# Kernel optimization log

Measured on AMD Instinct MI355X. Metric: run time of the kernel, lower is better.

Reference implementation:

```python
import jax, jax.numpy as jnp
import numpy as np

B, S, D, H = 2, 2048, 1024, 16
HD = D // H


def setup_inputs() -> dict:
    key = jax.random.key(0)
    ks = jax.random.split(key, 7)
    mk = lambda k, shape, scale=1.0: (jax.random.normal(k, shape, dtype=jnp.float32) * scale)
    w_scale = 1.0 / np.sqrt(D)  # ~nn.Linear init scale
    return {
        "query": mk(ks[0], (B, S, D)),
        "key": mk(ks[1], (B, S, D)),
        "value": mk(ks[2], (B, S, D)),
        "Wq": mk(ks[3], (D, D), w_scale),
        "Wk": mk(ks[4], (D, D), w_scale),
        "Wv": mk(ks[5], (D, D), w_scale),
        "Wo": mk(ks[6], (D, D), w_scale),
    }


def reference(query, key, value, Wq, Wk, Wv, Wo):
    # torch nn.Linear(bias=False): y = x @ W.T, W is (out, in)
    def proj(x, W):
        y = jnp.einsum('bsd,ed->bse', x, W)          # [B, S, D]
        return y.reshape(x.shape[0], x.shape[1], H, HD).transpose(0, 2, 1, 3)  # [B, H, S, HD]

    Q = proj(query, Wq)
    K = proj(key, Wk)
    V = proj(value, Wv)

    # NOTE: original scales by sqrt(embedding_size), not sqrt(head_dim)
    scale = 1.0 / jnp.sqrt(jnp.asarray(D, dtype=Q.dtype))
    scores = jnp.einsum('bhqd,bhkd->bhqk', Q, K) * scale   # [B, H, Q, K]
    attn = jax.nn.softmax(scores, axis=-1)
    ctx = jnp.einsum('bhqk,bhkd->bhqd', attn, V)           # [B, H, Q, HD]
    ctx = ctx.transpose(0, 2, 1, 3).reshape(query.shape[0], query.shape[1], D)
    return jnp.einsum('bsd,ed->bse', ctx, Wo)
```

## Files before the change

### kernel.cpp

```cpp
#include <hip/hip_runtime.h>
#include <hip/hip_bf16.h>


typedef __bf16 bf16x8 __attribute__((ext_vector_type(8)));
typedef float f32x2 __attribute__((ext_vector_type(2)));
typedef float f32x4 __attribute__((ext_vector_type(4)));
typedef float f32x8 __attribute__((ext_vector_type(8)));
typedef float f32x16 __attribute__((ext_vector_type(16)));
typedef int i32x4 __attribute__((ext_vector_type(4)));

static constexpr int Bb = 2, Ss = 2048, Dd = 1024, Hh = 16, HDd = 64;
static constexpr int Mtot = Bb * Ss;

__global__ __launch_bounds__(256) void cast_all(
    const float* __restrict__ a0, const float* __restrict__ a1, const float* __restrict__ a2,
    const float* __restrict__ a3, const float* __restrict__ a4, const float* __restrict__ a5,
    const float* __restrict__ a6, __hip_bfloat16* __restrict__ d0, __hip_bfloat16* __restrict__ d1,
    __hip_bfloat16* __restrict__ d2, __hip_bfloat16* __restrict__ d3,
    __hip_bfloat16* __restrict__ d4, __hip_bfloat16* __restrict__ d5,
    __hip_bfloat16* __restrict__ d6, int nact8, int nw8) {
  const float* src;
  __hip_bfloat16* dst;
  int n8;
  switch (blockIdx.y) {
    case 0: src = a0; dst = d0; n8 = nact8; break;
    case 1: src = a1; dst = d1; n8 = nact8; break;
    case 2: src = a2; dst = d2; n8 = nact8; break;
    case 3: src = a3; dst = d3; n8 = nw8; break;
    case 4: src = a4; dst = d4; n8 = nw8; break;
    case 5: src = a5; dst = d5; n8 = nw8; break;
    default: src = a6; dst = d6; n8 = nw8; break;
  }
  int i = blockIdx.x * 256 + threadIdx.x;
  if (i >= n8) return;
  const float4* s4 = (const float4*)src + (size_t)i * 2;
  float4 a = s4[0], b = s4[1];
  union { __hip_bfloat16 h[8]; int4 v; } u;
  u.h[0] = __float2bfloat16(a.x); u.h[1] = __float2bfloat16(a.y);
  u.h[2] = __float2bfloat16(a.z); u.h[3] = __float2bfloat16(a.w);
  u.h[4] = __float2bfloat16(b.x); u.h[5] = __float2bfloat16(b.y);
  u.h[6] = __float2bfloat16(b.z); u.h[7] = __float2bfloat16(b.w);
  ((int4*)dst)[i] = u.v;
}

#define BM 128
#define BK 64

__device__ __forceinline__ void gload_lds16(const void* g, void* l) {
  __builtin_amdgcn_global_load_lds((const __attribute__((address_space(1))) unsigned*)g,
                                   (__attribute__((address_space(3))) unsigned*)l, 16, 0, 0);
}

__device__ __forceinline__ void storeC(float* C, size_t idx, float v) { C[idx] = v; }
__device__ __forceinline__ void storeC(__hip_bfloat16* C, size_t idx, float v) {
  C[idx] = __float2bfloat16(v);
}

template <typename OutT, int BNT>
__device__ __forceinline__ void gemm_bt_body(const __hip_bfloat16* __restrict__ A,
                                             const __hip_bfloat16* __restrict__ Bw,
                                             OutT* __restrict__ C, int K, int N, float cscale) {
  constexpr int NTC = BNT / 32;
  __shared__ __hip_bfloat16 As[BM * BK];
  __shared__ __hip_bfloat16 Bs[BNT * BK];
  const int tid = threadIdx.x;
  const int lane = tid & 63;
  const int wid = tid >> 6;
  const int wm = (wid >> 1) * 64;
  const int wn = (wid & 1) * (BNT / 2);
  const int bm = blockIdx.x, bn = blockIdx.y;
  const int l15 = lane & 15;
  const int lhi = lane >> 4;

  f32x4 zero = {0.f, 0.f, 0.f, 0.f};
  f32x4 acc[4][NTC];
#pragma unroll
  for (int i = 0; i < 4; ++i)
#pragma unroll
    for (int j = 0; j < NTC; ++j) acc[i][j] = zero;

  const size_t abase = (size_t)(bm * BM) * K;
  const size_t bbase = (size_t)(bn * BNT) * K;

  for (int k0 = 0; k0 < K; k0 += BK) {
#pragma unroll
    for (int p = 0; p < 4; ++p) {
      int c = p * 256 + tid;
      int row = c >> 3;
      int col = (c & 7) * 8;
      gload_lds16(A + abase + (size_t)row * K + k0 + col, (char*)As + c * 16);
    }
#pragma unroll
    for (int p = 0; p < BNT / 32; ++p) {
      int c = p * 256 + tid;
      int row = c >> 3;
      int col = (c & 7) * 8;
      gload_lds16(Bw + bbase + (size_t)row * K + k0 + col, (char*)Bs + c * 16);
    }
    __syncthreads();
#pragma unroll
    for (int kk = 0; kk < 2; ++kk) {
      bf16x8 af[4], bfr[NTC];
#pragma unroll
      for (int mt = 0; mt < 4; ++mt)
        af[mt] = *(const bf16x8*)&As[(wm + mt * 16 + l15) * BK + kk * 32 + lhi * 8];
#pragma unroll
      for (int nt = 0; nt < NTC; ++nt)
        bfr[nt] = *(const bf16x8*)&Bs[(wn + nt * 16 + l15) * BK + kk * 32 + lhi * 8];
#pragma unroll
      for (int mt = 0; mt < 4; ++mt)
#pragma unroll
        for (int nt = 0; nt < NTC; ++nt)
          acc[mt][nt] = __builtin_amdgcn_mfma_f32_16x16x32_bf16(af[mt], bfr[nt], acc[mt][nt], 0, 0, 0);
    }
    __syncthreads();
  }

#pragma unroll
  for (int mt = 0; mt < 4; ++mt)
#pragma unroll
    for (int r = 0; r < 4; ++r) {
      int row = bm * BM + wm + mt * 16 + lhi * 4 + r;
#pragma unroll
      for (int nt = 0; nt < NTC; ++nt) {
        int col = bn * BNT + wn + nt * 16 + l15;
        storeC(C, (size_t)row * N + col, acc[mt][nt][r] * cscale);
      }
    }
}

__global__ __launch_bounds__(256) void qkv_proj(
    const __hip_bfloat16* __restrict__ xq, const __hip_bfloat16* __restrict__ xk,
    const __hip_bfloat16* __restrict__ xv, const __hip_bfloat16* __restrict__ wq,
    const __hip_bfloat16* __restrict__ wk, const __hip_bfloat16* __restrict__ wv,
    __hip_bfloat16* __restrict__ Qp, __hip_bfloat16* __restrict__ Kp,
    __hip_bfloat16* __restrict__ Vp) {
  const __hip_bfloat16* A;
  const __hip_bfloat16* W;
  __hip_bfloat16* C;
  float cs = 1.0f;
  if (blockIdx.z == 0) { A = xq; W = wq; C = Qp; cs = 0.04508422f; }
  else if (blockIdx.z == 1) { A = xk; W = wk; C = Kp; }
  else { A = xv; W = wv; C = Vp; }
  gemm_bt_body<__hip_bfloat16, 128>(A, W, C, Dd, Dd, cs);
}

__global__ __launch_bounds__(256) void out_proj(const __hip_bfloat16* __restrict__ ctx,
                                                const __hip_bfloat16* __restrict__ wo,
                                                float* __restrict__ out) {
  gemm_bt_body<float, 64>(ctx, wo, out, Dd, Dd, 1.0f);
}

__global__ __launch_bounds__(256) void transpose_v(const __hip_bfloat16* __restrict__ Vp,
                                                   __hip_bfloat16* __restrict__ Vt) {
  __shared__ __hip_bfloat16 T[64][72];
  const int tid = threadIdx.x;
  const int s0 = blockIdx.x * 64;
  const int bh = blockIdx.y;
  const int b = bh >> 4, h = bh & 15;
  const __hip_bfloat16* src = Vp + (size_t)b * Ss * Dd + (size_t)h * HDd;
#pragma unroll
  for (int p = 0; p < 2; ++p) {
    int id = p * 256 + tid;
    int r = id >> 3, c8 = (id & 7) * 8;
    *(int4*)&T[r][c8] = *(const int4*)(src + (size_t)(s0 + r) * Dd + c8);
  }
  __syncthreads();
#pragma unroll
  for (int p = 0; p < 2; ++p) {
    int id = p * 256 + tid;
    int d = id >> 3, s8 = (id & 7) * 8;
    union { int4 v; __hip_bfloat16 hh[8]; } u;
#pragma unroll
    for (int j = 0; j < 8; ++j) u.hh[j] = T[s8 + j][d];
    *(int4*)(Vt + ((size_t)bh * HDd + d) * Ss + s0 + s8) = u.v;
  }
}

__global__ __launch_bounds__(256) void attn_kernel(const __hip_bfloat16* __restrict__ Qp,
                                                   const __hip_bfloat16* __restrict__ Kp,
                                                   const __hip_bfloat16* __restrict__ Vt,
                                                   float* __restrict__ Po,
                                                   float* __restrict__ Pl) {
  constexpr int HT = 16;
  __shared__ __align__(16) __hip_bfloat16 Ks[3][64 * 64];
  __shared__ __align__(16) __hip_bfloat16 Vs[3][64 * 64];

  const int tid = threadIdx.x;
  const int lane = tid & 63, wid = tid >> 6;
  const int l31 = lane & 31;
  const bool hih = (lane >= 32);
  const int lhi2 = hih ? 1 : 0;

  const int bid = blockIdx.x;
  const int w = (bid & 7) * 128 + (bid >> 3);
  const int bh = w >> 5;
  const int qblk = (w & 31) >> 1;
  const int half = w & 1;

  const int b = bh >> 4, h = bh & 15;
  const size_t head_off = (size_t)b * Ss * Dd + (size_t)h * HDd;
  const size_t vt_off = (size_t)bh * HDd * Ss;
  const int qrow = qblk * 128 + wid * 32 + l31;

  bf16x8 qf[4];
#pragma unroll
  for (int ksd = 0; ksd < 4; ++ksd)
    qf[ksd] = *(const bf16x8*)(Qp + head_off + (size_t)qrow * Dd + ksd * 16 + lhi2 * 8);

  const i32x4 onesbits = {0x3F803F80, 0x3F803F80, 0x3F803F80, 0x3F803F80};
  const bf16x8 ones = __builtin_bit_cast(bf16x8, onesbits);

  f32x16 o[2], ol;
#pragma unroll
  for (int db = 0; db < 2; ++db)
#pragma unroll
    for (int r = 0; r < 16; ++r) o[db][r] = 0.f;
#pragma unroll
  for (int r = 0; r < 16; ++r) ol[r] = 0.f;

  auto stage = [&](int buf, int kv0) {
#pragma unroll
    for (int p = 0; p < 2; ++p) {
      int c = p * 256 + tid;
      int row = c >> 3;
      int sch = (c & 7) ^ (row & 7);
      gload_lds16(Kp + head_off + (size_t)(kv0 + row) * Dd + sch * 8,
                  (char*)&Ks[buf][0] + c * 16);
      gload_lds16(Vt + vt_off + (size_t)row * Ss + kv0 + sch * 8,
                  (char*)&Vs[buf][0] + c * 16);
    }
  };

  const int t0 = half * HT;
  stage(0, (t0 + 0) * 64);
  stage(1, (t0 + 1) * 64);
  asm volatile("s_waitcnt vmcnt(4)" ::: "memory");
  __builtin_amdgcn_s_barrier();
  __builtin_amdgcn_sched_barrier(0);

  int cur = 0;
  for (int t = 0; t < HT; ++t) {
    int sbuf = cur + 2; if (sbuf >= 3) sbuf -= 3;
    if (t + 2 < HT) stage(sbuf, (t0 + t + 2) * 64);

    const char* kbase = (const char*)&Ks[cur][0];
    bf16x8 kfrag[2][4];
#pragma unroll
    for (int kb = 0; kb < 2; ++kb) {
      int row = kb * 32 + l31;
#pragma unroll
      for (int ksd = 0; ksd < 4; ++ksd)
        kfrag[kb][ksd] = *(const bf16x8*)(kbase + row * 128 +
                                          (((ksd * 2 + lhi2) ^ (row & 7)) << 4));
    }
    f32x16 st[2];
#pragma unroll
    for (int kb = 0; kb < 2; ++kb)
#pragma unroll
      for (int r = 0; r < 16; ++r) st[kb][r] = 0.f;
    __builtin_amdgcn_s_setprio(1);
#pragma unroll
    for (int kb = 0; kb < 2; ++kb)
#pragma unroll
      for (int ksd = 0; ksd < 4; ++ksd)
        st[kb] = __builtin_amdgcn_mfma_f32_32x32x16_bf16(kfrag[kb][ksd], qf[ksd], st[kb], 0, 0, 0);
    __builtin_amdgcn_s_setprio(0);

#pragma unroll
    for (int kb = 0; kb < 2; ++kb)
#pragma unroll
      for (int r = 0; r < 16; ++r) st[kb][r] = exp2f(st[kb][r]);

    int cpk[2][4][2];
#pragma unroll
    for (int kb = 0; kb < 2; ++kb)
#pragma unroll
      for (int g = 0; g < 4; ++g)
#pragma unroll
        for (int i = 0; i < 2; ++i) {
          int rr;
          float lo = st[kb][g * 4 + 2 * i], hi = st[kb][g * 4 + 2 * i + 1];
          asm("v_cvt_pk_bf16_f32 %0, %1, %2" : "=v"(rr) : "v"(lo), "v"(hi));
          cpk[kb][g][i] = rr;
        }

    int own[2][2][2], rcv[2][2][2];
#pragma unroll
    for (int kb = 0; kb < 2; ++kb)
#pragma unroll
      for (int m = 0; m < 2; ++m)
#pragma unroll
        for (int i = 0; i < 2; ++i) {
          int cA = cpk[kb][2 * m][i];
          int cB = cpk[kb][2 * m + 1][i];
          int pay = hih ? cA : cB;
          own[kb][m][i] = hih ? cB : cA;
          rcv[kb][m][i] = __shfl_xor(pay, 32);
        }

    const char* vbase = (const char*)&Vs[cur][0];
    bf16x8 vfrag[4][2];
#pragma unroll
    for (int ks = 0; ks < 4; ++ks)
#pragma unroll
      for (int db = 0; db < 2; ++db) {
        int row = db * 32 + l31;
        vfrag[ks][db] = *(const bf16x8*)(vbase + row * 128 +
                                         (((ks * 2 + lhi2) ^ (row & 7)) << 4));
      }
    __builtin_amdgcn_s_setprio(1);
#pragma unroll
    for (int ks = 0; ks < 4; ++ks) {
      const int kb = ks >> 1, m = ks & 1;
      int w0 = hih ? rcv[kb][m][0] : own[kb][m][0];
      int w1 = hih ? rcv[kb][m][1] : own[kb][m][1];
      int w2 = hih ? own[kb][m][0] : rcv[kb][m][0];
      int w3 = hih ? own[kb][m][1] : rcv[kb][m][1];
      i32x4 bw = {w0, w1, w2, w3};
      bf16x8 pfrag = __builtin_bit_cast(bf16x8, bw);
#pragma unroll
      for (int db = 0; db < 2; ++db)
        o[db] = __builtin_amdgcn_mfma_f32_32x32x16_bf16(vfrag[ks][db], pfrag, o[db], 0, 0, 0);
      ol = __builtin_amdgcn_mfma_f32_32x32x16_bf16(ones, pfrag, ol, 0, 0, 0);
    }
    __builtin_amdgcn_s_setprio(0);

    if (t + 1 < HT) {
      if (t + 2 < HT) {
        asm volatile("s_waitcnt vmcnt(4)" ::: "memory");
      } else {
        asm volatile("s_waitcnt vmcnt(0)" ::: "memory");
      }
      __builtin_amdgcn_s_barrier();
      __builtin_amdgcn_sched_barrier(0);
    }
    cur = (cur == 2) ? 0 : cur + 1;
  }

  const int qlocal = wid * 32 + l31;
  float* prow = Po + (size_t)w * (128 * 64) + (size_t)qlocal * 64;
#pragma unroll
  for (int db = 0; db < 2; ++db)
#pragma unroll
    for (int g = 0; g < 4; ++g) {
      f32x4 v4 = {o[db][g * 4 + 0], o[db][g * 4 + 1], o[db][g * 4 + 2], o[db][g * 4 + 3]};
      *(f32x4*)(prow + db * 32 + 8 * g + 4 * lhi2) = v4;
    }
  if (!hih) Pl[(size_t)w * 128 + qlocal] = ol[0];
}

__global__ __launch_bounds__(256) void merge_halves(const float* __restrict__ Po,
                                                    const float* __restrict__ Pl,
                                                    __hip_bfloat16* __restrict__ ctx) {
  const int mb = blockIdx.x;
  const int bh = mb >> 4, qblk = mb & 15;
  const int b = bh >> 4, h = bh & 15;
  const int tid = threadIdx.x;
  const int q = tid >> 1;
  const int dh = (tid & 1) * 32;
  const size_t w0 = (size_t)bh * 32 + qblk * 2;
  const float* p0 = Po + w0 * (128 * 64) + (size_t)q * 64 + dh;
  const float* p1 = p0 + 128 * 64;
  float l = Pl[w0 * 128 + q] + Pl[w0 * 128 + 128 + q];
  float inv = 1.f / l;
  __hip_bfloat16* dst =
      ctx + (size_t)b * Ss * Dd + (size_t)(qblk * 128 + q) * Dd + h * HDd + dh;
#pragma unroll
  for (int j = 0; j < 32; j += 4) {
    f32x4 a = *(const f32x4*)(p0 + j);
    f32x4 c = *(const f32x4*)(p1 + j);
    f32x4 s = (a + c) * inv;
    union { uint2 v; __hip_bfloat16 hh[4]; } u;
#pragma unroll
    for (int k = 0; k < 4; ++k) u.hh[k] = __float2bfloat16(s[k]);
    *(uint2*)(dst + j) = u.v;
  }
}

extern "C" void kernel_launch(void* const* d_in, const int* in_sizes, int n_in,
                              void* d_out, int out_size, void* d_ws, size_t ws_size,
                              hipStream_t stream) {
  const float* q_f = (const float*)d_in[0];
  const float* k_f = (const float*)d_in[1];
  const float* v_f = (const float*)d_in[2];
  const float* wq_f = (const float*)d_in[3];
  const float* wk_f = (const float*)d_in[4];
  const float* wv_f = (const float*)d_in[5];
  const float* wo_f = (const float*)d_in[6];
  float* out = (float*)d_out;

  const size_t act = (size_t)Mtot * Dd;
  const size_t wsz = (size_t)Dd * Dd;
  char* ws = (char*)d_ws;

  __hip_bfloat16* Qp = (__hip_bfloat16*)ws;   ws += act * 2;
  __hip_bfloat16* Kp = (__hip_bfloat16*)ws;   ws += act * 2;
  __hip_bfloat16* Vt = (__hip_bfloat16*)ws;   ws += act * 2;
  __hip_bfloat16* ctxb = (__hip_bfloat16*)ws; ws += act * 2;
  __hip_bfloat16* wob = (__hip_bfloat16*)ws;  ws += wsz * 2;

  char* scratch = ws;
  __hip_bfloat16* qb = (__hip_bfloat16*)scratch;
  __hip_bfloat16* kb = qb + act;
  __hip_bfloat16* vb = kb + act;
  __hip_bfloat16* wqb = vb + act;
  __hip_bfloat16* wkb = wqb + wsz;
  __hip_bfloat16* wvb = wkb + wsz;
  __hip_bfloat16* Vp = wvb + wsz;

  float* Po = (float*)scratch;
  float* Pl = Po + (size_t)1024 * 128 * 64;

  dim3 gc((unsigned)(act / 8 / 256), 7);
  cast_all<<<gc, 256, 0, stream>>>(q_f, k_f, v_f, wq_f, wk_f, wv_f, wo_f, qb, kb, vb, wqb,
                                   wkb, wvb, wob, (int)(act / 8), (int)(wsz / 8));

  dim3 gq(Mtot / BM, Dd / 128, 3);
  qkv_proj<<<gq, 256, 0, stream>>>(qb, kb, vb, wqb, wkb, wvb, Qp, Kp, Vp);

  dim3 gt(Ss / 64, Bb * Hh);
  transpose_v<<<gt, 256, 0, stream>>>(Vp, Vt);

  attn_kernel<<<1024, 256, 0, stream>>>(Qp, Kp, Vt, Po, Pl);

  merge_halves<<<512, 256, 0, stream>>>(Po, Pl, ctxb);

  dim3 go(Mtot / BM, Dd / 64);
  out_proj<<<go, 256, 0, stream>>>(ctxb, wob, out);
}
```

Measured before the change: 173.3 us.

## Drop LDS staging in attention; single-wave blocks load K/V directly from global

After: 231.8 us. +33.7%, slower.

```diff
diff --git a/kernel.cpp b/kernel.cpp
--- a/kernel.cpp
+++ b/kernel.cpp
@@ -177,100 +177,89 @@
   }
 }
 
-__global__ __launch_bounds__(256) void attn_kernel(const __hip_bfloat16* __restrict__ Qp,
-                                                   const __hip_bfloat16* __restrict__ Kp,
-                                                   const __hip_bfloat16* __restrict__ Vt,
-                                                   float* __restrict__ Po,
-                                                   float* __restrict__ Pl) {
+__global__ __launch_bounds__(64, 4) void attn_kernel(const __hip_bfloat16* __restrict__ Qp,
+                                                     const __hip_bfloat16* __restrict__ Kp,
+                                                     const __hip_bfloat16* __restrict__ Vt,
+                                                     float* __restrict__ Po,
+                                                     float* __restrict__ Pl) {
   constexpr int HT = 16;
-  __shared__ __align__(16) __hip_bfloat16 Ks[3][64 * 64];
-  __shared__ __align__(16) __hip_bfloat16 Vs[3][64 * 64];
-
-  const int tid = threadIdx.x;
-  const int lane = tid & 63, wid = tid >> 6;
+  const int lane = threadIdx.x & 63;
   const int l31 = lane & 31;
   const bool hih = (lane >= 32);
   const int lhi2 = hih ? 1 : 0;
 
   const int bid = blockIdx.x;
-  const int w = (bid & 7) * 128 + (bid >> 3);
-  const int bh = w >> 5;
-  const int qblk = (w & 31) >> 1;
+  const int w = (bid & 7) * 512 + (bid >> 3);
+  const int bh = w >> 7;
+  const int qw = (w & 127) >> 1;
   const int half = w & 1;
 
   const int b = bh >> 4, h = bh & 15;
   const size_t head_off = (size_t)b * Ss * Dd + (size_t)h * HDd;
   const size_t vt_off = (size_t)bh * HDd * Ss;
-  const int qrow = qblk * 128 + wid * 32 + l31;
+  const int qrow = qw * 32 + l31;
 
   bf16x8 qf[4];
 #pragma unroll
   for (int ksd = 0; ksd < 4; ++ksd)
     qf[ksd] = *(const bf16x8*)(Qp + head_off + (size_t)qrow * Dd + ksd * 16 + lhi2 * 8);
 
-  const i32x4 onesbits = {0x3F803F80, 0x3F803F80, 0x3F803F80, 0x3F803F80};
-  const bf16x8 ones = __builtin_bit_cast(bf16x8, onesbits);
-
-  f32x16 o[2], ol;
+  float l_run = 0.f;
+  f32x16 o[2];
 #pragma unroll
   for (int db = 0; db < 2; ++db)
 #pragma unroll
     for (int r = 0; r < 16; ++r) o[db][r] = 0.f;
-#pragma unroll
-  for (int r = 0; r < 16; ++r) ol[r] = 0.f;
-
-  auto stage = [&](int buf, int kv0) {
-#pragma unroll
-    for (int p = 0; p < 2; ++p) {
-      int c = p * 256 + tid;
-      int row = c >> 3;
-      int sch = (c & 7) ^ (row & 7);
-      gload_lds16(Kp + head_off + (size_t)(kv0 + row) * Dd + sch * 8,
-                  (char*)&Ks[buf][0] + c * 16);
-      gload_lds16(Vt + vt_off + (size_t)row * Ss + kv0 + sch * 8,
-                  (char*)&Vs[buf][0] + c * 16);
-    }
-  };
-
-  const int t0 = half * HT;
-  stage(0, (t0 + 0) * 64);
-  stage(1, (t0 + 1) * 64);
-  asm volatile("s_waitcnt vmcnt(4)" ::: "memory");
-  __builtin_amdgcn_s_barrier();
-  __builtin_amdgcn_sched_barrier(0);
-
-  int cur = 0;
+
+  const __hip_bfloat16* kbase =
+      Kp + head_off + ((size_t)half * 1024 + l31) * Dd + lhi2 * 8;
+  const __hip_bfloat16* vbase =
+      Vt + vt_off + (size_t)l31 * Ss + half * 1024 + lhi2 * 8;
+
   for (int t = 0; t < HT; ++t) {
-    int sbuf = cur + 2; if (sbuf >= 3) sbuf -= 3;
-    if (t + 2 < HT) stage(sbuf, (t0 + t + 2) * 64);
-
-    const char* kbase = (const char*)&Ks[cur][0];
+    const int kv0 = t * 64;
+
     bf16x8 kfrag[2][4];
 #pragma unroll
-    for (int kb = 0; kb < 2; ++kb) {
-      int row = kb * 32 + l31;
+    for (int kb = 0; kb < 2; ++kb)
 #pragma unroll
       for (int ksd = 0; ksd < 4; ++ksd)
-        kfrag[kb][ksd] = *(const bf16x8*)(kbase + row * 128 +
-                                          (((ksd * 2 + lhi2) ^ (row & 7)) << 4));
-    }
+        kfrag[kb][ksd] =
+            *(const bf16x8*)(kbase + (size_t)(kv0 + kb * 32) * Dd + ksd * 16);
+
+    bf16x8 vfrag[4][2];
+#pragma unroll
+    for (int ks = 0; ks < 4; ++ks)
+#pragma unroll
+      for (int db = 0; db < 2; ++db)
+        vfrag[ks][db] =
+            *(const bf16x8*)(vbase + (size_t)(db * 32) * Ss + kv0 + ks * 16);
+
     f32x16 st[2];
 #pragma unroll
     for (int kb = 0; kb < 2; ++kb)
 #pragma unroll
       for (int r = 0; r < 16; ++r) st[kb][r] = 0.f;
-    __builtin_amdgcn_s_setprio(1);
 #pragma unroll
     for (int kb = 0; kb < 2; ++kb)
 #pragma unroll
       for (int ksd = 0; ksd < 4; ++ksd)
         st[kb] = __builtin_amdgcn_mfma_f32_32x32x16_bf16(kfrag[kb][ksd], qf[ksd], st[kb], 0, 0, 0);
-    __builtin_amdgcn_s_setprio(0);
 
 #pragma unroll
     for (int kb = 0; kb < 2; ++kb)
 #pragma unroll
       for (int r = 0; r < 16; ++r) st[kb][r] = exp2f(st[kb][r]);
+
+    f32x16 s16 = st[0] + st[1];
+    f32x8 s8 = __builtin_shufflevector(s16, s16, 0, 1, 2, 3, 4, 5, 6, 7) +
+               __builtin_shufflevector(s16, s16, 8, 9, 10, 11, 12, 13, 14, 15);
+    f32x4 s4 = __builtin_shufflevector(s8, s8, 0, 1, 2, 3) +
+               __builtin_shufflevector(s8, s8, 4, 5, 6, 7);
+    f32x2 s2 = __builtin_shufflevector(s4, s4, 0, 1) + __builtin_shufflevector(s4, s4, 2, 3);
+    float ps = s2[0] + s2[1];
+    ps += __shfl_xor(ps, 32);
+    l_run += ps;
 
     int cpk[2][4][2];
 #pragma unroll
@@ -299,17 +288,6 @@
           rcv[kb][m][i] = __shfl_xor(pay, 32);
         }
 
-    const char* vbase = (const char*)&Vs[cur][0];
-    bf16x8 vfrag[4][2];
-#pragma unroll
-    for (int ks = 0; ks < 4; ++ks)
-#pragma unroll
-      for (int db = 0; db < 2; ++db) {
-        int row = db * 32 + l31;
-        vfrag[ks][db] = *(const bf16x8*)(vbase + row * 128 +
-                                         (((ks * 2 + lhi2) ^ (row & 7)) << 4));
-      }
-    __builtin_amdgcn_s_setprio(1);
 #pragma unroll
     for (int ks = 0; ks < 4; ++ks) {
       const int kb = ks >> 1, m = ks & 1;
@@ -322,24 +300,10 @@
 #pragma unroll
       for (int db = 0; db < 2; ++db)
         o[db] = __builtin_amdgcn_mfma_f32_32x32x16_bf16(vfrag[ks][db], pfrag, o[db], 0, 0, 0);
-      ol = __builtin_amdgcn_mfma_f32_32x32x16_bf16(ones, pfrag, ol, 0, 0, 0);
-    }
-    __builtin_amdgcn_s_setprio(0);
-
-    if (t + 1 < HT) {
-      if (t + 2 < HT) {
-        asm volatile("s_waitcnt vmcnt(4)" ::: "memory");
-      } else {
-        asm volatile("s_waitcnt vmcnt(0)" ::: "memory");
-      }
-      __builtin_amdgcn_s_barrier();
-      __builtin_amdgcn_sched_barrier(0);
-    }
-    cur = (cur == 2) ? 0 : cur + 1;
-  }
-
-  const int qlocal = wid * 32 + l31;
-  float* prow = Po + (size_t)w * (128 * 64) + (size_t)qlocal * 64;
+    }
+  }
+
+  float* prow = Po + (size_t)w * (32 * 64) + (size_t)l31 * 64;
 #pragma unroll
   for (int db = 0; db < 2; ++db)
 #pragma unroll
@@ -347,7 +311,7 @@
       f32x4 v4 = {o[db][g * 4 + 0], o[db][g * 4 + 1], o[db][g * 4 + 2], o[db][g * 4 + 3]};
       *(f32x4*)(prow + db * 32 + 8 * g + 4 * lhi2) = v4;
     }
-  if (!hih) Pl[(size_t)w * 128 + qlocal] = ol[0];
+  if (!hih) Pl[(size_t)w * 32 + l31] = l_run;
 }
 
 __global__ __launch_bounds__(256) void merge_halves(const float* __restrict__ Po,
@@ -359,10 +323,12 @@
   const int tid = threadIdx.x;
   const int q = tid >> 1;
   const int dh = (tid & 1) * 32;
-  const size_t w0 = (size_t)bh * 32 + qblk * 2;
-  const float* p0 = Po + w0 * (128 * 64) + (size_t)q * 64 + dh;
-  const float* p1 = p0 + 128 * 64;
-  float l = Pl[w0 * 128 + q] + Pl[w0 * 128 + 128 + q];
+  const int qw = qblk * 4 + (q >> 5);
+  const int ql = q & 31;
+  const size_t w0 = (size_t)bh * 128 + qw * 2;
+  const float* p0 = Po + w0 * (32 * 64) + (size_t)ql * 64 + dh;
+  const float* p1 = p0 + 32 * 64;
+  float l = Pl[w0 * 32 + ql] + Pl[w0 * 32 + 32 + ql];
   float inv = 1.f / l;
   __hip_bfloat16* dst =
       ctx + (size_t)b * Ss * Dd + (size_t)(qblk * 128 + q) * Dd + h * HDd + dh;
@@ -410,7 +376,7 @@
   __hip_bfloat16* Vp = wvb + wsz;
 
   float* Po = (float*)scratch;
-  float* Pl = Po + (size_t)1024 * 128 * 64;
+  float* Pl = Po + (size_t)4096 * 32 * 64;
 
   dim3 gc((unsigned)(act / 8 / 256), 7);
   cast_all<<<gc, 256, 0, stream>>>(q_f, k_f, v_f, wq_f, wk_f, wv_f, wo_f, qb, kb, vb, wqb,
@@ -422,7 +388,7 @@
   dim3 gt(Ss / 64, Bb * Hh);
   transpose_v<<<gt, 256, 0, stream>>>(Vp, Vt);
 
-  attn_kernel<<<1024, 256, 0, stream>>>(Qp, Kp, Vt, Po, Pl);
+  attn_kernel<<<4096, 64, 0, stream>>>(Qp, Kp, Vt, Po, Pl);
 
   merge_halves<<<512, 256, 0, stream>>>(Po, Pl, ctxb);
 
```

## Double-buffer K/V with split waits and compute row sums on VALU

Applied to the files above, without the earlier changes.

Result: faster. 158.8 us (-8.4%).

```diff
diff --git a/kernel.cpp b/kernel.cpp
--- a/kernel.cpp
+++ b/kernel.cpp
@@ -177,14 +177,14 @@
   }
 }
 
-__global__ __launch_bounds__(256) void attn_kernel(const __hip_bfloat16* __restrict__ Qp,
-                                                   const __hip_bfloat16* __restrict__ Kp,
-                                                   const __hip_bfloat16* __restrict__ Vt,
-                                                   float* __restrict__ Po,
-                                                   float* __restrict__ Pl) {
+__global__ __launch_bounds__(256, 4) void attn_kernel(const __hip_bfloat16* __restrict__ Qp,
+                                                      const __hip_bfloat16* __restrict__ Kp,
+                                                      const __hip_bfloat16* __restrict__ Vt,
+                                                      float* __restrict__ Po,
+                                                      float* __restrict__ Pl) {
   constexpr int HT = 16;
-  __shared__ __align__(16) __hip_bfloat16 Ks[3][64 * 64];
-  __shared__ __align__(16) __hip_bfloat16 Vs[3][64 * 64];
+  __shared__ __align__(16) __hip_bfloat16 Ks[2][64 * 64];
+  __shared__ __align__(16) __hip_bfloat16 Vs[2][64 * 64];
 
   const int tid = threadIdx.x;
   const int lane = tid & 63, wid = tid >> 6;
@@ -208,18 +208,14 @@
   for (int ksd = 0; ksd < 4; ++ksd)
     qf[ksd] = *(const bf16x8*)(Qp + head_off + (size_t)qrow * Dd + ksd * 16 + lhi2 * 8);
 
-  const i32x4 onesbits = {0x3F803F80, 0x3F803F80, 0x3F803F80, 0x3F803F80};
-  const bf16x8 ones = __builtin_bit_cast(bf16x8, onesbits);
-
-  f32x16 o[2], ol;
+  float l_run = 0.f;
+  f32x16 o[2];
 #pragma unroll
   for (int db = 0; db < 2; ++db)
 #pragma unroll
     for (int r = 0; r < 16; ++r) o[db][r] = 0.f;
-#pragma unroll
-  for (int r = 0; r < 16; ++r) ol[r] = 0.f;
-
-  auto stage = [&](int buf, int kv0) {
+
+  auto stage_K = [&](int buf, int kv0) {
 #pragma unroll
     for (int p = 0; p < 2; ++p) {
       int c = p * 256 + tid;
@@ -227,22 +223,34 @@
       int sch = (c & 7) ^ (row & 7);
       gload_lds16(Kp + head_off + (size_t)(kv0 + row) * Dd + sch * 8,
                   (char*)&Ks[buf][0] + c * 16);
+    }
+  };
+  auto stage_V = [&](int buf, int kv0) {
+#pragma unroll
+    for (int p = 0; p < 2; ++p) {
+      int c = p * 256 + tid;
+      int row = c >> 3;
+      int sch = (c & 7) ^ (row & 7);
       gload_lds16(Vt + vt_off + (size_t)row * Ss + kv0 + sch * 8,
                   (char*)&Vs[buf][0] + c * 16);
     }
   };
 
   const int t0 = half * HT;
-  stage(0, (t0 + 0) * 64);
-  stage(1, (t0 + 1) * 64);
+  stage_K(0, (t0 + 0) * 64);
+  stage_V(0, (t0 + 0) * 64);
+  stage_K(1, (t0 + 1) * 64);
+  stage_V(1, (t0 + 1) * 64);
   asm volatile("s_waitcnt vmcnt(4)" ::: "memory");
   __builtin_amdgcn_s_barrier();
   __builtin_amdgcn_sched_barrier(0);
 
-  int cur = 0;
   for (int t = 0; t < HT; ++t) {
-    int sbuf = cur + 2; if (sbuf >= 3) sbuf -= 3;
-    if (t + 2 < HT) stage(sbuf, (t0 + t + 2) * 64);
+    const int cur = t & 1;
+    if (t > 0 && t + 1 < HT) {
+      stage_K(cur ^ 1, (t0 + t + 1) * 64);
+      stage_V(cur ^ 1, (t0 + t + 1) * 64);
+    }
 
     const char* kbase = (const char*)&Ks[cur][0];
     bf16x8 kfrag[2][4];
@@ -271,6 +279,16 @@
     for (int kb = 0; kb < 2; ++kb)
 #pragma unroll
       for (int r = 0; r < 16; ++r) st[kb][r] = exp2f(st[kb][r]);
+
+    f32x16 s16 = st[0] + st[1];
+    f32x8 s8 = __builtin_shufflevector(s16, s16, 0, 1, 2, 3, 4, 5, 6, 7) +
+               __builtin_shufflevector(s16, s16, 8, 9, 10, 11, 12, 13, 14, 15);
+    f32x4 s4 = __builtin_shufflevector(s8, s8, 0, 1, 2, 3) +
+               __builtin_shufflevector(s8, s8, 4, 5, 6, 7);
+    f32x2 s2 = __builtin_shufflevector(s4, s4, 0, 1) + __builtin_shufflevector(s4, s4, 2, 3);
+    float ps = s2[0] + s2[1];
+    ps += __shfl_xor(ps, 32);
+    l_run += ps;
 
     int cpk[2][4][2];
 #pragma unroll
@@ -298,6 +316,12 @@
           own[kb][m][i] = hih ? cB : cA;
           rcv[kb][m][i] = __shfl_xor(pay, 32);
         }
+
+    if (t + 1 < HT) {
+      asm volatile("s_waitcnt vmcnt(4)" ::: "memory");
+    } else {
+      asm volatile("s_waitcnt vmcnt(0)" ::: "memory");
+    }
 
     const char* vbase = (const char*)&Vs[cur][0];
     bf16x8 vfrag[4][2];
@@ -322,20 +346,14 @@
 #pragma unroll
       for (int db = 0; db < 2; ++db)
         o[db] = __builtin_amdgcn_mfma_f32_32x32x16_bf16(vfrag[ks][db], pfrag, o[db], 0, 0, 0);
-      ol = __builtin_amdgcn_mfma_f32_32x32x16_bf16(ones, pfrag, ol, 0, 0, 0);
     }
     __builtin_amdgcn_s_setprio(0);
 
     if (t + 1 < HT) {
-      if (t + 2 < HT) {
-        asm volatile("s_waitcnt vmcnt(4)" ::: "memory");
-      } else {
-        asm volatile("s_waitcnt vmcnt(0)" ::: "memory");
-      }
+      asm volatile("s_waitcnt vmcnt(2)" ::: "memory");
       __builtin_amdgcn_s_barrier();
       __builtin_amdgcn_sched_barrier(0);
     }
-    cur = (cur == 2) ? 0 : cur + 1;
   }
 
   const int qlocal = wid * 32 + l31;
@@ -347,7 +365,7 @@
       f32x4 v4 = {o[db][g * 4 + 0], o[db][g * 4 + 1], o[db][g * 4 + 2], o[db][g * 4 + 3]};
       *(f32x4*)(prow + db * 32 + 8 * g + 4 * lhi2) = v4;
     }
-  if (!hih) Pl[(size_t)w * 128 + qlocal] = ol[0];
+  if (!hih) Pl[(size_t)w * 128 + qlocal] = l_run;
 }
 
 __global__ __launch_bounds__(256) void merge_halves(const float* __restrict__ Po,
```
